# Kernel tuning notes

Measured on AMD Instinct MI355X. Metric: run time of the kernel, lower is better.

## Reference

```python
import jax, jax.numpy as jnp
import numpy as np

EPS = 1e-5  # torch LayerNorm default eps

def _ln(x, g, b):
    mu = jnp.mean(x, axis=-1, keepdims=True)
    var = jnp.mean((x - mu) ** 2, axis=-1, keepdims=True)
    return (x - mu) * jax.lax.rsqrt(var + EPS) * g + b

def setup_inputs() -> dict:
    key = jax.random.key(0)
    ks = jax.random.split(key, 8)
    B, N, F, E, H = 8, 512, 64, 16, 4
    node = jax.random.normal(ks[0], (B, N, F), jnp.float32)
    edge = jax.random.normal(ks[1], (B, N, N, E), jnp.float32)
    adj = jax.random.randint(ks[2], (B, N, N), 0, 2, jnp.int32)
    s = lambda k, shp, fan: jax.random.normal(k, shp, jnp.float32) / np.sqrt(fan).astype(np.float32)
    return dict(
        node=node, edge=edge, adj=adj,
        ln1_g=jnp.ones((F,), jnp.float32), ln1_b=jnp.zeros((F,), jnp.float32),
        Wn=s(ks[3], (F, F), F), bn=jnp.zeros((F,), jnp.float32),
        ln2_g=jnp.ones((E,), jnp.float32), ln2_b=jnp.zeros((E,), jnp.float32),
        We1=s(ks[4], (2 * E, E), E), be1=jnp.zeros((2 * E,), jnp.float32),
        We2=s(ks[5], (E, 2 * E), 2 * E), be2=jnp.zeros((E,), jnp.float32),
        lne_g=jnp.ones((E,), jnp.float32), lne_b=jnp.zeros((E,), jnp.float32),
        attn_A=s(ks[6], (H, 2 * (F // H) + E), F // H),
        Wo=s(ks[7], (F, F), F), bo=jnp.zeros((F,), jnp.float32),
        lno_g=jnp.ones((F,), jnp.float32), lno_b=jnp.zeros((F,), jnp.float32),
    )

def reference(node, edge, adj, ln1_g, ln1_b, Wn, bn, ln2_g, ln2_b, We1, be1, We2, be2, lne_g, lne_b, attn_A, Wo, bo, lno_g, lno_b):
    B, N, F = node.shape
    H = attn_A.shape[0]
    hd = F // H
    node_res = node
    # node projection (dropout = identity at eval)
    h = _ln(node, ln1_g, ln1_b) @ Wn.T + bn                         # (B,N,F)
    # edge MLP with residual + layer norm
    e = _ln(edge, ln2_g, ln2_b)
    e = jax.nn.celu(e @ We1.T + be1) @ We2.T + be2
    e = _ln(e + edge, lne_g, lne_b)                                  # (B,N,N,E)
    h = h.reshape(B, N, H, hd)
    # (concat @ attn_matrix.T).sum(-1) == concat . attn_matrix.sum(0)
    a = attn_A.sum(0)                                                # (2*hd+E,)
    a_row, a_col, a_edge = a[:hd], a[hd:2 * hd], a[2 * hd:]
    sr = jnp.einsum('bnhx,x->bnh', h, a_row)                         # row term (b,i,h)
    sc = jnp.einsum('bnhx,x->bnh', h, a_col)                         # col term (b,j,h)
    se = jnp.einsum('bije,e->bij', e, a_edge)                        # edge term (b,i,j)
    logits = sr[:, :, None, :] + sc[:, None, :, :] + se[..., None]   # (B,N,N,H)
    logits = jnp.where(adj[..., None] == 0, jnp.float32(-1e9), logits)
    logits = jax.nn.leaky_relu(logits, 0.2)
    logits = jnp.clip(logits, -1e9, 1e9)
    coeffs = jax.nn.softmax(logits, axis=2)                          # softmax over j
    coeffs = jnp.nan_to_num(coeffs, nan=0.0)
    # msg[b,n,h,x] = sum_m h[b,m,h,x] * coeffs[b,n,m,h]
    msg = jnp.einsum('bmhx,bnmh->bnhx', h, coeffs).reshape(B, N, F)
    out = msg @ Wo.T + bo + node_res                                 # residual_proj == Identity (in==out)
    out = jax.nn.leaky_relu(out, 0.2)
    out = _ln(out, lno_g, lno_b)
    return (out, e, adj)
```

## Files before the change

kernel.cpp:

```cpp
#include <hip/hip_runtime.h>

#define EPS 1e-5f

typedef __attribute__((ext_vector_type(8))) short bfrag;
typedef __attribute__((ext_vector_type(4))) float ffrag;

union BFU { int i[4]; bfrag v; };

__device__ __forceinline__ float wave_sum64(float v) {
    #pragma unroll
    for (int off = 32; off > 0; off >>= 1) v += __shfl_xor(v, off, 64);
    return v;
}
__device__ __forceinline__ float wave_max64(float v) {
    #pragma unroll
    for (int off = 32; off > 0; off >>= 1) v = fmaxf(v, __shfl_xor(v, off, 64));
    return v;
}

__device__ __forceinline__ int pk_bf16(float a, float b) {
    union { float f; unsigned u; } x, y;
    x.f = a; y.f = b;
    unsigned ra = (x.u + 0x7fffu + ((x.u >> 16) & 1u)) >> 16;
    unsigned rb = (y.u + 0x7fffu + ((y.u >> 16) & 1u)) >> 16;
    return (int)((rb << 16) | (ra & 0xffffu));
}

__device__ __forceinline__ float qsum(float v) {
    v += __shfl_xor(v, 16, 64);
    v += __shfl_xor(v, 32, 64);
    return v;
}

__device__ __forceinline__ float celu1(float x) {
    return (x > 0.f) ? x : (__expf(x) - 1.f);
}

__global__ __launch_bounds__(64) void node_kernel(
    const float* __restrict__ node, const float* __restrict__ ln1_g, const float* __restrict__ ln1_b,
    const float* __restrict__ Wn, const float* __restrict__ bn, const float* __restrict__ attn_A,
    float* __restrict__ h_out, float* __restrict__ sr_out, float* __restrict__ sc_out)
{
    const int row  = blockIdx.x;
    const int lane = threadIdx.x;

    float x = node[(long)row * 64 + lane];
    float mu  = wave_sum64(x) * (1.0f / 64.0f);
    float d   = x - mu;
    float var = wave_sum64(d * d) * (1.0f / 64.0f);
    float xln = d * rsqrtf(var + EPS) * ln1_g[lane] + ln1_b[lane];

    __shared__ float xs[64];
    xs[lane] = xln;
    __syncthreads();

    float acc = bn[lane];
    const float* wrow = Wn + lane * 64;
    #pragma unroll
    for (int f = 0; f < 64; ++f) acc = fmaf(xs[f], wrow[f], acc);
    h_out[(long)row * 64 + lane] = acc;

    const int xidx = lane & 15;
    float ar = 0.f, ac = 0.f;
    #pragma unroll
    for (int hh = 0; hh < 4; ++hh) {
        ar += attn_A[hh * 48 + xidx];
        ac += attn_A[hh * 48 + 16 + xidx];
    }
    float pr = acc * ar, pc = acc * ac;
    #pragma unroll
    for (int off = 8; off > 0; off >>= 1) {
        pr += __shfl_down(pr, off, 16);
        pc += __shfl_down(pc, off, 16);
    }
    if (xidx == 0) {
        const int head = lane >> 4;
        sr_out[(long)row * 4 + head] = pr;
        sc_out[(long)row * 4 + head] = pc;
    }
}

__global__ __launch_bounds__(256, 4) void edge_kernel(
    const float* __restrict__ edge, const int* __restrict__ adj,
    const float* __restrict__ ln2_g, const float* __restrict__ ln2_b,
    const float* __restrict__ We1, const float* __restrict__ be1,
    const float* __restrict__ We2, const float* __restrict__ be2,
    const float* __restrict__ lne_g, const float* __restrict__ lne_b,
    const float* __restrict__ attn_A,
    float* __restrict__ e_out, float* __restrict__ adj_out, float* __restrict__ se_out)
{
    const int tid  = threadIdx.x;
    const int wave = tid >> 6;
    const int lane = tid & 63;
    const int q    = lane >> 4;
    const int t    = lane & 15;
    const long r0  = (long)blockIdx.x * 256 + wave * 64;
    const int  c4  = 4 * q;

    const float4 g1  = *(const float4*)(ln2_g + c4);
    const float4 b1  = *(const float4*)(ln2_b + c4);
    const float4 gE  = *(const float4*)(lne_g + c4);
    const float4 bE  = *(const float4*)(lne_b + c4);
    const float4 vb2 = *(const float4*)(be2 + c4);
    const float4 vb1a = *(const float4*)(be1 + 8 * q);
    const float4 vb1b = *(const float4*)(be1 + 8 * q + 4);
    float4 ae = make_float4(0.f, 0.f, 0.f, 0.f);
    #pragma unroll
    for (int hh = 0; hh < 4; ++hh) {
        float4 a = *(const float4*)(attn_A + hh * 48 + 32 + c4);
        ae.x += a.x; ae.y += a.y; ae.z += a.z; ae.w += a.w;
    }

    BFU A1[2], A2;
    A1[0].i[0] = A1[0].i[1] = A1[0].i[2] = A1[0].i[3] = 0;
    A1[1].i[0] = A1[1].i[1] = A1[1].i[2] = A1[1].i[3] = 0;
    if (q < 2) {
        const int rr = 8 * (t >> 2) + (t & 3);
        #pragma unroll
        for (int mt = 0; mt < 2; ++mt) {
            const float* wp = We1 + (rr + 4 * mt) * 16 + 8 * q;
            float4 w0 = *(const float4*)(wp);
            float4 w1 = *(const float4*)(wp + 4);
            A1[mt].i[0] = pk_bf16(w0.x, w0.y);
            A1[mt].i[1] = pk_bf16(w0.z, w0.w);
            A1[mt].i[2] = pk_bf16(w1.x, w1.y);
            A1[mt].i[3] = pk_bf16(w1.z, w1.w);
        }
    }
    {
        const float* wp = We2 + t * 32 + 8 * q;
        float4 w0 = *(const float4*)(wp);
        float4 w1 = *(const float4*)(wp + 4);
        A2.i[0] = pk_bf16(w0.x, w0.y);
        A2.i[1] = pk_bf16(w0.z, w0.w);
        A2.i[2] = pk_bf16(w1.x, w1.y);
        A2.i[3] = pk_bf16(w1.z, w1.w);
    }

    const int srcA = ((q & 1) << 5) + t;
    const int srcB = srcA + 16;

    #pragma unroll
    for (int nt = 0; nt < 4; ++nt) {
        const long R = r0 + 16 * nt + t;
        const float4 v = *(const float4*)(edge + R * 16 + c4);

        float s1 = v.x + v.y + v.z + v.w;
        float s2 = fmaf(v.x, v.x, fmaf(v.y, v.y, fmaf(v.z, v.z, v.w * v.w)));
        s1 = qsum(s1);
        s2 = qsum(s2);
        const float mu = s1 * (1.0f / 16.0f);
        float var = fmaxf(s2 * (1.0f / 16.0f) - mu * mu, 0.f);
        const float rs = rsqrtf(var + EPS);
        const float x0 = (v.x - mu) * rs * g1.x + b1.x;
        const float x1 = (v.y - mu) * rs * g1.y + b1.y;
        const float x2 = (v.z - mu) * rs * g1.z + b1.z;
        const float x3 = (v.w - mu) * rs * g1.w + b1.w;
        const int p0 = pk_bf16(x0, x1), p1 = pk_bf16(x2, x3);

        BFU B1;
        B1.i[0] = __shfl(p0, srcA, 64);
        B1.i[1] = __shfl(p1, srcA, 64);
        B1.i[2] = __shfl(p0, srcB, 64);
        B1.i[3] = __shfl(p1, srcB, 64);

        ffrag acc0 = { vb1a.x, vb1a.y, vb1a.z, vb1a.w };
        ffrag acc1 = { vb1b.x, vb1b.y, vb1b.z, vb1b.w };
        acc0 = __builtin_amdgcn_mfma_f32_16x16x32_bf16(A1[0].v, B1.v, acc0, 0, 0, 0);
        acc1 = __builtin_amdgcn_mfma_f32_16x16x32_bf16(A1[1].v, B1.v, acc1, 0, 0, 0);

        BFU B2;
        B2.i[0] = pk_bf16(celu1(acc0[0]), celu1(acc0[1]));
        B2.i[1] = pk_bf16(celu1(acc0[2]), celu1(acc0[3]));
        B2.i[2] = pk_bf16(celu1(acc1[0]), celu1(acc1[1]));
        B2.i[3] = pk_bf16(celu1(acc1[2]), celu1(acc1[3]));

        ffrag acc2 = { vb2.x, vb2.y, vb2.z, vb2.w };
        acc2 = __builtin_amdgcn_mfma_f32_16x16x32_bf16(A2.v, B2.v, acc2, 0, 0, 0);

        const float o0 = acc2[0] + v.x;
        const float o1 = acc2[1] + v.y;
        const float o2 = acc2[2] + v.z;
        const float o3 = acc2[3] + v.w;
        float m1 = o0 + o1 + o2 + o3;
        float m2 = fmaf(o0, o0, fmaf(o1, o1, fmaf(o2, o2, o3 * o3)));
        m1 = qsum(m1);
        m2 = qsum(m2);
        const float mu2 = m1 * (1.0f / 16.0f);
        float var2 = fmaxf(m2 * (1.0f / 16.0f) - mu2 * mu2, 0.f);
        const float rs2 = rsqrtf(var2 + EPS);
        const float e0 = (o0 - mu2) * rs2 * gE.x + bE.x;
        const float e1 = (o1 - mu2) * rs2 * gE.y + bE.y;
        const float e2 = (o2 - mu2) * rs2 * gE.z + bE.z;
        const float e3 = (o3 - mu2) * rs2 * gE.w + bE.w;

        *(float4*)(e_out + R * 16 + c4) = make_float4(e0, e1, e2, e3);

        float sep = fmaf(e0, ae.x, fmaf(e1, ae.y, fmaf(e2, ae.z, e3 * ae.w)));
        sep = qsum(sep);
        if (q == 0) se_out[R] = sep;
    }

    adj_out[r0 + lane] = (float)adj[r0 + lane];
}

#define G 4
__global__ __launch_bounds__(256, 4) void attn_kernel(
    const float* __restrict__ h_ws, const float* __restrict__ sr_ws, const float* __restrict__ sc_ws,
    const float* __restrict__ se_ws, const int* __restrict__ adj,
    const float* __restrict__ node, const float* __restrict__ Wo, const float* __restrict__ bo,
    const float* __restrict__ lno_g, const float* __restrict__ lno_b,
    float* __restrict__ out)
{
    const int bi0  = blockIdx.x * G;
    const int b    = bi0 >> 9;
    const int tid  = threadIdx.x;
    const int wave = tid >> 6;
    const int lane = tid & 63;

    __shared__ __align__(16) float coef[G][4][516];
    __shared__ float hpart[4][G][64];
    __shared__ float msg_s[G][64];

    const float4* sc4 = (const float4*)(sc_ws + (long)b * 512 * 4);

    #pragma unroll
    for (int r = 0; r < G; ++r) {
        const int row = bi0 + r;
        const float sr0 = sr_ws[(long)row * 4 + 0];
        const float sr1 = sr_ws[(long)row * 4 + 1];
        const float sr2 = sr_ws[(long)row * 4 + 2];
        const float sr3 = sr_ws[(long)row * 4 + 3];
        const float* se_row  = se_ws + (long)row * 512;
        const int*   adj_row = adj   + (long)row * 512;
        #pragma unroll
        for (int half = 0; half < 2; ++half) {
            const int j = half * 256 + tid;
            float4 s = sc4[j];
            float  se = se_row[j];
            bool   m  = (adj_row[j] != 0);
            float l0 = m ? (sr0 + s.x + se) : -1e9f;
            float l1 = m ? (sr1 + s.y + se) : -1e9f;
            float l2 = m ? (sr2 + s.z + se) : -1e9f;
            float l3 = m ? (sr3 + s.w + se) : -1e9f;
            l0 = (l0 > 0.f) ? l0 : 0.2f * l0;  l0 = fminf(fmaxf(l0, -1e9f), 1e9f);
            l1 = (l1 > 0.f) ? l1 : 0.2f * l1;  l1 = fminf(fmaxf(l1, -1e9f), 1e9f);
            l2 = (l2 > 0.f) ? l2 : 0.2f * l2;  l2 = fminf(fmaxf(l2, -1e9f), 1e9f);
            l3 = (l3 > 0.f) ? l3 : 0.2f * l3;  l3 = fminf(fmaxf(l3, -1e9f), 1e9f);
            coef[r][0][j] = l0; coef[r][1][j] = l1; coef[r][2][j] = l2; coef[r][3][j] = l3;
        }
    }
    __syncthreads();

    #pragma unroll
    for (int qq = 0; qq < 4; ++qq) {
        const int p = qq * 4 + wave;
        float* L = coef[p >> 2][p & 3];
        float4 va = *(const float4*)&L[lane * 8];
        float4 vb = *(const float4*)&L[lane * 8 + 4];
        float m = fmaxf(fmaxf(fmaxf(va.x, va.y), fmaxf(va.z, va.w)),
                        fmaxf(fmaxf(vb.x, vb.y), fmaxf(vb.z, vb.w)));
        m = wave_max64(m);
        va.x = __expf(va.x - m); va.y = __expf(va.y - m);
        va.z = __expf(va.z - m); va.w = __expf(va.w - m);
        vb.x = __expf(vb.x - m); vb.y = __expf(vb.y - m);
        vb.z = __expf(vb.z - m); vb.w = __expf(vb.w - m);
        float s = (va.x + va.y + va.z + va.w) + (vb.x + vb.y + vb.z + vb.w);
        s = wave_sum64(s);
        const float inv = 1.0f / s;
        va.x *= inv; va.y *= inv; va.z *= inv; va.w *= inv;
        vb.x *= inv; vb.y *= inv; vb.z *= inv; vb.w *= inv;
        *(float4*)&L[lane * 8]     = va;
        *(float4*)&L[lane * 8 + 4] = vb;
    }
    __syncthreads();

    {
        const int head = lane >> 4;
        const float* hb = h_ws + (long)b * 512 * 64;
        float a0 = 0.f, a1 = 0.f, a2 = 0.f, a3 = 0.f;
        const int j0 = wave * 128;
        #pragma unroll 2
        for (int j = j0; j < j0 + 128; j += 4) {
            float4 c0 = *(const float4*)&coef[0][head][j];
            float4 c1 = *(const float4*)&coef[1][head][j];
            float4 c2 = *(const float4*)&coef[2][head][j];
            float4 c3 = *(const float4*)&coef[3][head][j];
            float h0v = hb[(long)(j + 0) * 64 + lane];
            float h1v = hb[(long)(j + 1) * 64 + lane];
            float h2v = hb[(long)(j + 2) * 64 + lane];
            float h3v = hb[(long)(j + 3) * 64 + lane];
            a0 = fmaf(h3v, c0.w, fmaf(h2v, c0.z, fmaf(h1v, c0.y, fmaf(h0v, c0.x, a0))));
            a1 = fmaf(h3v, c1.w, fmaf(h2v, c1.z, fmaf(h1v, c1.y, fmaf(h0v, c1.x, a1))));
            a2 = fmaf(h3v, c2.w, fmaf(h2v, c2.z, fmaf(h1v, c2.y, fmaf(h0v, c2.x, a2))));
            a3 = fmaf(h3v, c3.w, fmaf(h2v, c3.z, fmaf(h1v, c3.y, fmaf(h0v, c3.x, a3))));
        }
        hpart[wave][0][lane] = a0;
        hpart[wave][1][lane] = a1;
        hpart[wave][2][lane] = a2;
        hpart[wave][3][lane] = a3;
    }
    __syncthreads();

    {
        const int r   = wave;
        const int row = bi0 + r;
        float m = hpart[0][r][lane] + hpart[1][r][lane] + hpart[2][r][lane] + hpart[3][r][lane];
        msg_s[r][lane] = m;

        float o = bo[lane];
        const float* wrow = Wo + lane * 64;
        #pragma unroll
        for (int ff = 0; ff < 64; ++ff) o = fmaf(msg_s[r][ff], wrow[ff], o);
        o += node[(long)row * 64 + lane];
        o = (o > 0.f) ? o : 0.2f * o;
        float mu  = wave_sum64(o) * (1.0f / 64.0f);
        float d   = o - mu;
        float var = wave_sum64(d * d) * (1.0f / 64.0f);
        out[(long)row * 64 + lane] = d * rsqrtf(var + EPS) * lno_g[lane] + lno_b[lane];
    }
}

extern "C" void kernel_launch(void* const* d_in, const int* in_sizes, int n_in,
                              void* d_out, int out_size, void* d_ws, size_t ws_size,
                              hipStream_t stream) {
    const float* node   = (const float*)d_in[0];
    const float* edge   = (const float*)d_in[1];
    const int*   adj    = (const int*)  d_in[2];
    const float* ln1_g  = (const float*)d_in[3];
    const float* ln1_b  = (const float*)d_in[4];
    const float* Wn     = (const float*)d_in[5];
    const float* bn     = (const float*)d_in[6];
    const float* ln2_g  = (const float*)d_in[7];
    const float* ln2_b  = (const float*)d_in[8];
    const float* We1    = (const float*)d_in[9];
    const float* be1    = (const float*)d_in[10];
    const float* We2    = (const float*)d_in[11];
    const float* be2    = (const float*)d_in[12];
    const float* lne_g  = (const float*)d_in[13];
    const float* lne_b  = (const float*)d_in[14];
    const float* attn_A = (const float*)d_in[15];
    const float* Wo     = (const float*)d_in[16];
    const float* bo     = (const float*)d_in[17];
    const float* lno_g  = (const float*)d_in[18];
    const float* lno_b  = (const float*)d_in[19];

    float* out_p  = (float*)d_out;
    float* e_out  = out_p + 262144;
    float* adj_o  = e_out + 33554432;

    float* ws    = (float*)d_ws;
    float* h_ws  = ws;
    float* sr_ws = ws + 262144;
    float* sc_ws = ws + 278528;
    float* se_ws = ws + 294912;

    node_kernel<<<4096, 64, 0, stream>>>(node, ln1_g, ln1_b, Wn, bn, attn_A, h_ws, sr_ws, sc_ws);
    edge_kernel<<<8192, 256, 0, stream>>>(edge, adj, ln2_g, ln2_b, We1, be1, We2, be2,
                                          lne_g, lne_b, attn_A, e_out, adj_o, se_ws);
    attn_kernel<<<1024, 256, 0, stream>>>(h_ws, sr_ws, sc_ws, se_ws, adj, node,
                                          Wo, bo, lno_g, lno_b, out_p);
}
```

Before: 328.4 us.

## Restructure edge MLP so MFMA inputs come straight from loads, dropping shuffles

The edge kernel now has each lane load 8 contiguous edge features, so the packed bf16 LayerNorm output feeds the first MFMA directly instead of being redistributed with four cross-lane shuffles per row tile. Two 16-row groups are processed per iteration using split lo/hi weight fragments, and a permuted We2 row mapping plus a single xor-32 exchange realigns outputs for the residual LayerNorm. The intent is to cut shuffle traffic and reduction steps (one xor instead of two per statistic). In exchange it issues more MFMAs per row, half of which multiply zero-padded weight fragments, and adds some extra select logic.

```diff
diff --git a/kernel.cpp b/kernel.cpp
--- a/kernel.cpp
+++ b/kernel.cpp
@@ -24,12 +24,6 @@
     unsigned ra = (x.u + 0x7fffu + ((x.u >> 16) & 1u)) >> 16;
     unsigned rb = (y.u + 0x7fffu + ((y.u >> 16) & 1u)) >> 16;
     return (int)((rb << 16) | (ra & 0xffffu));
-}
-
-__device__ __forceinline__ float qsum(float v) {
-    v += __shfl_xor(v, 16, 64);
-    v += __shfl_xor(v, 32, 64);
-    return v;
 }
 
 __device__ __forceinline__ float celu1(float x) {
@@ -94,41 +88,65 @@
     const int lane = tid & 63;
     const int q    = lane >> 4;
     const int t    = lane & 15;
+    const int qq   = q & 1;
+    const int h    = q >> 1;
     const long r0  = (long)blockIdx.x * 256 + wave * 64;
-    const int  c4  = 4 * q;
-
-    const float4 g1  = *(const float4*)(ln2_g + c4);
-    const float4 b1  = *(const float4*)(ln2_b + c4);
-    const float4 gE  = *(const float4*)(lne_g + c4);
-    const float4 bE  = *(const float4*)(lne_b + c4);
-    const float4 vb2 = *(const float4*)(be2 + c4);
+    const int  c8  = 8 * qq;
+
+    const float4 g1a = *(const float4*)(ln2_g + c8);
+    const float4 g1b = *(const float4*)(ln2_g + c8 + 4);
+    const float4 b1a = *(const float4*)(ln2_b + c8);
+    const float4 b1b = *(const float4*)(ln2_b + c8 + 4);
+    const float4 gEa = *(const float4*)(lne_g + c8);
+    const float4 gEb = *(const float4*)(lne_g + c8 + 4);
+    const float4 bEa = *(const float4*)(lne_b + c8);
+    const float4 bEb = *(const float4*)(lne_b + c8 + 4);
+    float4 aea = make_float4(0.f, 0.f, 0.f, 0.f);
+    float4 aeb = make_float4(0.f, 0.f, 0.f, 0.f);
+    #pragma unroll
+    for (int hh = 0; hh < 4; ++hh) {
+        float4 a = *(const float4*)(attn_A + hh * 48 + 32 + c8);
+        float4 b = *(const float4*)(attn_A + hh * 48 + 32 + c8 + 4);
+        aea.x += a.x; aea.y += a.y; aea.z += a.z; aea.w += a.w;
+        aeb.x += b.x; aeb.y += b.y; aeb.z += b.z; aeb.w += b.w;
+    }
     const float4 vb1a = *(const float4*)(be1 + 8 * q);
     const float4 vb1b = *(const float4*)(be1 + 8 * q + 4);
-    float4 ae = make_float4(0.f, 0.f, 0.f, 0.f);
-    #pragma unroll
-    for (int hh = 0; hh < 4; ++hh) {
-        float4 a = *(const float4*)(attn_A + hh * 48 + 32 + c4);
-        ae.x += a.x; ae.y += a.y; ae.z += a.z; ae.w += a.w;
-    }
-
-    BFU A1[2], A2;
-    A1[0].i[0] = A1[0].i[1] = A1[0].i[2] = A1[0].i[3] = 0;
-    A1[1].i[0] = A1[1].i[1] = A1[1].i[2] = A1[1].i[3] = 0;
+    const float4 vb2c = *(const float4*)(be2 + c8 + 4 * h);
+
+    BFU A1lo[2], A1hi[2], A2;
+    #pragma unroll
+    for (int mt = 0; mt < 2; ++mt) {
+        A1lo[mt].i[0] = A1lo[mt].i[1] = A1lo[mt].i[2] = A1lo[mt].i[3] = 0;
+        A1hi[mt].i[0] = A1hi[mt].i[1] = A1hi[mt].i[2] = A1hi[mt].i[3] = 0;
+    }
+    const int rr = 8 * (t >> 2) + (t & 3);
     if (q < 2) {
-        const int rr = 8 * (t >> 2) + (t & 3);
         #pragma unroll
         for (int mt = 0; mt < 2; ++mt) {
             const float* wp = We1 + (rr + 4 * mt) * 16 + 8 * q;
             float4 w0 = *(const float4*)(wp);
             float4 w1 = *(const float4*)(wp + 4);
-            A1[mt].i[0] = pk_bf16(w0.x, w0.y);
-            A1[mt].i[1] = pk_bf16(w0.z, w0.w);
-            A1[mt].i[2] = pk_bf16(w1.x, w1.y);
-            A1[mt].i[3] = pk_bf16(w1.z, w1.w);
+            A1lo[mt].i[0] = pk_bf16(w0.x, w0.y);
+            A1lo[mt].i[1] = pk_bf16(w0.z, w0.w);
+            A1lo[mt].i[2] = pk_bf16(w1.x, w1.y);
+            A1lo[mt].i[3] = pk_bf16(w1.z, w1.w);
         }
+    } else {
+        #pragma unroll
+        for (int mt = 0; mt < 2; ++mt) {
+            const float* wp = We1 + (rr + 4 * mt) * 16 + 8 * (q - 2);
+            float4 w0 = *(const float4*)(wp);
+            float4 w1 = *(const float4*)(wp + 4);
+            A1hi[mt].i[0] = pk_bf16(w0.x, w0.y);
+            A1hi[mt].i[1] = pk_bf16(w0.z, w0.w);
+            A1hi[mt].i[2] = pk_bf16(w1.x, w1.y);
+            A1hi[mt].i[3] = pk_bf16(w1.z, w1.w);
+        }
     }
     {
-        const float* wp = We2 + t * 32 + 8 * q;
+        const int cht = 8 * ((t >> 2) & 1) + 4 * (t >> 3) + (t & 3);
+        const float* wp = We2 + cht * 32 + 8 * q;
         float4 w0 = *(const float4*)(wp);
         float4 w1 = *(const float4*)(wp + 4);
         A2.i[0] = pk_bf16(w0.x, w0.y);
@@ -137,68 +155,96 @@
         A2.i[3] = pk_bf16(w1.z, w1.w);
     }
 
-    const int srcA = ((q & 1) << 5) + t;
-    const int srcB = srcA + 16;
-
-    #pragma unroll
-    for (int nt = 0; nt < 4; ++nt) {
-        const long R = r0 + 16 * nt + t;
-        const float4 v = *(const float4*)(edge + R * 16 + c4);
-
-        float s1 = v.x + v.y + v.z + v.w;
-        float s2 = fmaf(v.x, v.x, fmaf(v.y, v.y, fmaf(v.z, v.z, v.w * v.w)));
-        s1 = qsum(s1);
-        s2 = qsum(s2);
+    #pragma unroll
+    for (int nt = 0; nt < 2; ++nt) {
+        const long row = r0 + 32 * nt + 16 * h + t;
+        const float* ep = edge + row * 16 + c8;
+        const float4 va = *(const float4*)(ep);
+        const float4 vb = *(const float4*)(ep + 4);
+
+        float s1 = (va.x + va.y + va.z + va.w) + (vb.x + vb.y + vb.z + vb.w);
+        float s2 = fmaf(va.x, va.x, fmaf(va.y, va.y, fmaf(va.z, va.z, va.w * va.w)));
+        s2 = fmaf(vb.x, vb.x, fmaf(vb.y, vb.y, fmaf(vb.z, vb.z, fmaf(vb.w, vb.w, s2))));
+        s1 += __shfl_xor(s1, 16, 64);
+        s2 += __shfl_xor(s2, 16, 64);
         const float mu = s1 * (1.0f / 16.0f);
         float var = fmaxf(s2 * (1.0f / 16.0f) - mu * mu, 0.f);
         const float rs = rsqrtf(var + EPS);
-        const float x0 = (v.x - mu) * rs * g1.x + b1.x;
-        const float x1 = (v.y - mu) * rs * g1.y + b1.y;
-        const float x2 = (v.z - mu) * rs * g1.z + b1.z;
-        const float x3 = (v.w - mu) * rs * g1.w + b1.w;
-        const int p0 = pk_bf16(x0, x1), p1 = pk_bf16(x2, x3);
-
-        BFU B1;
-        B1.i[0] = __shfl(p0, srcA, 64);
-        B1.i[1] = __shfl(p1, srcA, 64);
-        B1.i[2] = __shfl(p0, srcB, 64);
-        B1.i[3] = __shfl(p1, srcB, 64);
-
-        ffrag acc0 = { vb1a.x, vb1a.y, vb1a.z, vb1a.w };
-        ffrag acc1 = { vb1b.x, vb1b.y, vb1b.z, vb1b.w };
-        acc0 = __builtin_amdgcn_mfma_f32_16x16x32_bf16(A1[0].v, B1.v, acc0, 0, 0, 0);
-        acc1 = __builtin_amdgcn_mfma_f32_16x16x32_bf16(A1[1].v, B1.v, acc1, 0, 0, 0);
-
-        BFU B2;
-        B2.i[0] = pk_bf16(celu1(acc0[0]), celu1(acc0[1]));
-        B2.i[1] = pk_bf16(celu1(acc0[2]), celu1(acc0[3]));
-        B2.i[2] = pk_bf16(celu1(acc1[0]), celu1(acc1[1]));
-        B2.i[3] = pk_bf16(celu1(acc1[2]), celu1(acc1[3]));
-
-        ffrag acc2 = { vb2.x, vb2.y, vb2.z, vb2.w };
-        acc2 = __builtin_amdgcn_mfma_f32_16x16x32_bf16(A2.v, B2.v, acc2, 0, 0, 0);
-
-        const float o0 = acc2[0] + v.x;
-        const float o1 = acc2[1] + v.y;
-        const float o2 = acc2[2] + v.z;
-        const float o3 = acc2[3] + v.w;
-        float m1 = o0 + o1 + o2 + o3;
+        const float x0 = (va.x - mu) * rs * g1a.x + b1a.x;
+        const float x1 = (va.y - mu) * rs * g1a.y + b1a.y;
+        const float x2 = (va.z - mu) * rs * g1a.z + b1a.z;
+        const float x3 = (va.w - mu) * rs * g1a.w + b1a.w;
+        const float x4 = (vb.x - mu) * rs * g1b.x + b1b.x;
+        const float x5 = (vb.y - mu) * rs * g1b.y + b1b.y;
+        const float x6 = (vb.z - mu) * rs * g1b.z + b1b.z;
+        const float x7 = (vb.w - mu) * rs * g1b.w + b1b.w;
+
+        BFU p;
+        p.i[0] = pk_bf16(x0, x1);
+        p.i[1] = pk_bf16(x2, x3);
+        p.i[2] = pk_bf16(x4, x5);
+        p.i[3] = pk_bf16(x6, x7);
+
+        ffrag a00 = { vb1a.x, vb1a.y, vb1a.z, vb1a.w };
+        ffrag a01 = { vb1b.x, vb1b.y, vb1b.z, vb1b.w };
+        ffrag a10 = { vb1a.x, vb1a.y, vb1a.z, vb1a.w };
+        ffrag a11 = { vb1b.x, vb1b.y, vb1b.z, vb1b.w };
+        a00 = __builtin_amdgcn_mfma_f32_16x16x32_bf16(A1lo[0].v, p.v, a00, 0, 0, 0);
+        a01 = __builtin_amdgcn_mfma_f32_16x16x32_bf16(A1lo[1].v, p.v, a01, 0, 0, 0);
+        a10 = __builtin_amdgcn_mfma_f32_16x16x32_bf16(A1hi[0].v, p.v, a10, 0, 0, 0);
+        a11 = __builtin_amdgcn_mfma_f32_16x16x32_bf16(A1hi[1].v, p.v, a11, 0, 0, 0);
+
+        BFU B20, B21;
+        B20.i[0] = pk_bf16(celu1(a00[0]), celu1(a00[1]));
+        B20.i[1] = pk_bf16(celu1(a00[2]), celu1(a00[3]));
+        B20.i[2] = pk_bf16(celu1(a01[0]), celu1(a01[1]));
+        B20.i[3] = pk_bf16(celu1(a01[2]), celu1(a01[3]));
+        B21.i[0] = pk_bf16(celu1(a10[0]), celu1(a10[1]));
+        B21.i[1] = pk_bf16(celu1(a10[2]), celu1(a10[3]));
+        B21.i[2] = pk_bf16(celu1(a11[0]), celu1(a11[1]));
+        B21.i[3] = pk_bf16(celu1(a11[2]), celu1(a11[3]));
+
+        ffrag d0 = { vb2c.x, vb2c.y, vb2c.z, vb2c.w };
+        ffrag d1 = { vb2c.x, vb2c.y, vb2c.z, vb2c.w };
+        d0 = __builtin_amdgcn_mfma_f32_16x16x32_bf16(A2.v, B20.v, d0, 0, 0, 0);
+        d1 = __builtin_amdgcn_mfma_f32_16x16x32_bf16(A2.v, B21.v, d1, 0, 0, 0);
+
+        const float ex0 = __shfl_xor(h ? d0[0] : d1[0], 32, 64);
+        const float ex1 = __shfl_xor(h ? d0[1] : d1[1], 32, 64);
+        const float ex2 = __shfl_xor(h ? d0[2] : d1[2], 32, 64);
+        const float ex3 = __shfl_xor(h ? d0[3] : d1[3], 32, 64);
+        const float l0 = h ? ex0 : d0[0], l1 = h ? ex1 : d0[1];
+        const float l2 = h ? ex2 : d0[2], l3 = h ? ex3 : d0[3];
+        const float u0 = h ? d1[0] : ex0, u1 = h ? d1[1] : ex1;
+        const float u2 = h ? d1[2] : ex2, u3 = h ? d1[3] : ex3;
+
+        const float o0 = l0 + va.x, o1 = l1 + va.y, o2 = l2 + va.z, o3 = l3 + va.w;
+        const float o4 = u0 + vb.x, o5 = u1 + vb.y, o6 = u2 + vb.z, o7 = u3 + vb.w;
+        float m1 = (o0 + o1 + o2 + o3) + (o4 + o5 + o6 + o7);
         float m2 = fmaf(o0, o0, fmaf(o1, o1, fmaf(o2, o2, o3 * o3)));
-        m1 = qsum(m1);
-        m2 = qsum(m2);
+        m2 = fmaf(o4, o4, fmaf(o5, o5, fmaf(o6, o6, fmaf(o7, o7, m2))));
+        m1 += __shfl_xor(m1, 16, 64);
+        m2 += __shfl_xor(m2, 16, 64);
         const float mu2 = m1 * (1.0f / 16.0f);
         float var2 = fmaxf(m2 * (1.0f / 16.0f) - mu2 * mu2, 0.f);
         const float rs2 = rsqrtf(var2 + EPS);
-        const float e0 = (o0 - mu2) * rs2 * gE.x + bE.x;
-        const float e1 = (o1 - mu2) * rs2 * gE.y + bE.y;
-        const float e2 = (o2 - mu2) * rs2 * gE.z + bE.z;
-        const float e3 = (o3 - mu2) * rs2 * gE.w + bE.w;
-
-        *(float4*)(e_out + R * 16 + c4) = make_float4(e0, e1, e2, e3);
-
-        float sep = fmaf(e0, ae.x, fmaf(e1, ae.y, fmaf(e2, ae.z, e3 * ae.w)));
-        sep = qsum(sep);
-        if (q == 0) se_out[R] = sep;
+        const float e0 = (o0 - mu2) * rs2 * gEa.x + bEa.x;
+        const float e1 = (o1 - mu2) * rs2 * gEa.y + bEa.y;
+        const float e2 = (o2 - mu2) * rs2 * gEa.z + bEa.z;
+        const float e3 = (o3 - mu2) * rs2 * gEa.w + bEa.w;
+        const float e4 = (o4 - mu2) * rs2 * gEb.x + bEb.x;
+        const float e5 = (o5 - mu2) * rs2 * gEb.y + bEb.y;
+        const float e6 = (o6 - mu2) * rs2 * gEb.z + bEb.z;
+        const float e7 = (o7 - mu2) * rs2 * gEb.w + bEb.w;
+
+        float* op = e_out + row * 16 + c8;
+        *(float4*)(op)     = make_float4(e0, e1, e2, e3);
+        *(float4*)(op + 4) = make_float4(e4, e5, e6, e7);
+
+        float sep = fmaf(e0, aea.x, fmaf(e1, aea.y, fmaf(e2, aea.z, e3 * aea.w)));
+        sep = fmaf(e4, aeb.x, fmaf(e5, aeb.y, fmaf(e6, aeb.z, fmaf(e7, aeb.w, sep))));
+        sep += __shfl_xor(sep, 16, 64);
+        if (qq == 0) se_out[row] = sep;
     }
 
     adj_out[r0 + lane] = (float)adj[r0 + lane];
```

Result: slower. 339.4 us (+3.3%).
